# Kernel optimization log

Measured on AMD Instinct MI355X. Metric: run time of the kernel, lower is better.

## Reference

```python
import jax, jax.numpy as jnp
import numpy as np

B, H, W, C = 32, 112, 112, 192
K = 7  # spatial attention conv kernel size


def setup_inputs() -> dict:
    key = jax.random.key(0)
    k1, k2 = jax.random.split(key)
    x = jax.random.normal(k1, (B, H, W, C), dtype=jnp.float32)
    # he_normal init for 7x7 conv with 2 input channels, 1 output channel (HWIO)
    fan_in = K * K * 2
    conv_w = jax.random.normal(k2, (K, K, 2, 1), dtype=jnp.float32) * jnp.sqrt(2.0 / fan_in)
    return {"x": x, "conv_w": conv_w}


def reference(x, conv_w):
    # channel-wise reductions: [B,H,W,1] each
    avg_out = jnp.mean(x, axis=-1, keepdims=True)
    max_out = jnp.max(x, axis=-1, keepdims=True)
    concat = jnp.concatenate([avg_out, max_out], axis=-1)  # [B,H,W,2]
    # 7x7 conv, stride 1, SAME padding, no bias -> [B,H,W,1]
    att = jax.lax.conv_general_dilated(
        concat, conv_w,
        window_strides=(1, 1), padding="SAME",
        dimension_numbers=("NHWC", "HWIO", "NHWC"),
    )
    att = jax.nn.sigmoid(att)
    return x * att  # broadcast multiply back onto full feature map
```

## Files before the change

### kernel.cpp

```cpp
#include <hip/hip_runtime.h>
#include <math.h>

#define B_ 32
#define H_ 112
#define W_ 112
#define C_ 192
#define C4 (C_/4)
#define R_ 7
#define TPI (H_/R_)
#define NBLK (B_*TPI)
#define HALO 3
#define SR (R_ + 2*HALO)
#define SW (W_ + 2*HALO)
#define SWP 120
#define NT_ 1024

typedef float nf4 __attribute__((ext_vector_type(4)));

__global__ __launch_bounds__(NT_, 8) void fused_kernel(const float* __restrict__ x,
                                                       const float* __restrict__ w,
                                                       float* __restrict__ out) {
    __shared__ float2 sm[SR][SWP];
    __shared__ float  sw[98];
    __shared__ float  satt[R_ * W_];

    const int tid = threadIdx.x;
    const int bid = ((int)blockIdx.x & 7) * (NBLK / 8) + ((int)blockIdx.x >> 3);
    const int b   = bid / TPI;
    const int t   = bid - b * TPI;
    const int y0  = t * R_;

    if (tid < 98) sw[tid] = w[tid];
    for (int i = tid; i < SR * SWP; i += NT_)
        ((float2*)sm)[i] = make_float2(0.0f, 0.0f);
    __syncthreads();

    const int g   = tid >> 4;
    const int sub = tid & 15;
    const float* xbase = x + (size_t)(b * H_) * W_ * C_;
    for (int j = 0; j < (SR * W_ + 63) / 64; ++j) {
        const int ps = j * 64 + g;
        if (ps < SR * W_) {
            const int r  = ps / W_;
            const int cl = ps - r * W_;
            const int yy = y0 + r - HALO;
            if (yy >= 0 && yy < H_) {
                const nf4* xp = (const nf4*)(xbase + ((size_t)yy * W_ + cl) * C_);
                nf4 a0 = xp[sub];
                nf4 a1 = xp[sub + 16];
                nf4 a2 = xp[sub + 32];
                float s = ((a0[0]+a0[1]) + (a0[2]+a0[3]))
                        + ((a1[0]+a1[1]) + (a1[2]+a1[3]))
                        + ((a2[0]+a2[1]) + (a2[2]+a2[3]));
                float m0 = fmaxf(fmaxf(a0[0], a0[1]), fmaxf(a0[2], a0[3]));
                float m1 = fmaxf(fmaxf(a1[0], a1[1]), fmaxf(a1[2], a1[3]));
                float m2 = fmaxf(fmaxf(a2[0], a2[1]), fmaxf(a2[2], a2[3]));
                float m  = fmaxf(m0, fmaxf(m1, m2));
                #pragma unroll
                for (int off = 8; off > 0; off >>= 1) {
                    s += __shfl_xor(s, off);
                    m = fmaxf(m, __shfl_xor(m, off));
                }
                if (sub == 0)
                    sm[r][HALO + cl] = make_float2(s * (1.0f / (float)C_), m);
            }
        }
    }
    __syncthreads();

    if (tid < R_ * W_) {
        const int r  = tid / W_;
        const int cl = tid - r * W_;
        float acc = 0.0f;
        #pragma unroll
        for (int ky = 0; ky < 7; ++ky) {
            #pragma unroll
            for (int kx = 0; kx < 7; ++kx) {
                float2 am = sm[r + ky][cl + kx];
                acc = fmaf(am.x, sw[(ky * 7 + kx) * 2 + 0], acc);
                acc = fmaf(am.y, sw[(ky * 7 + kx) * 2 + 1], acc);
            }
        }
        satt[tid] = 1.0f / (1.0f + __expf(-acc));
    }
    __syncthreads();

    const size_t base4 = (size_t)(b * H_ + y0) * W_ * C4;
    const nf4* xr   = (const nf4*)x + base4;
    nf4*       orow = (nf4*)out + base4;
    for (int f = tid; f < R_ * W_ * C4; f += NT_) {
        nf4 v = xr[f];
        v = v * satt[f / C4];
        __builtin_nontemporal_store(v, &orow[f]);
    }
}

extern "C" void kernel_launch(void* const* d_in, const int* in_sizes, int n_in,
                              void* d_out, int out_size, void* d_ws, size_t ws_size,
                              hipStream_t stream) {
    const float* x = (const float*)d_in[0];
    const float* w = (const float*)d_in[1];
    float* out = (float*)d_out;
    fused_kernel<<<NBLK, NT_, 0, stream>>>(x, w, out);
}
```

Before: 173.6 us.

## Split into reduce and apply phases with grid sync to drop halo recompute

```diff
diff --git a/kernel.cpp b/kernel.cpp
--- a/kernel.cpp
+++ b/kernel.cpp
@@ -1,74 +1,86 @@
 #include <hip/hip_runtime.h>
+#include <hip/hip_cooperative_groups.h>
 #include <math.h>
+
+namespace cg = cooperative_groups;
 
 #define B_ 32
 #define H_ 112
 #define W_ 112
 #define C_ 192
 #define C4 (C_/4)
-#define R_ 7
-#define TPI (H_/R_)
-#define NBLK (B_*TPI)
+#define NPOS (B_*H_*W_)
+#define NBLK 1792
+#define RPI (H_/2)
 #define HALO 3
-#define SR (R_ + 2*HALO)
-#define SW (W_ + 2*HALO)
 #define SWP 120
-#define NT_ 1024
 
 typedef float nf4 __attribute__((ext_vector_type(4)));
 
-__global__ __launch_bounds__(NT_, 8) void fused_kernel(const float* __restrict__ x,
-                                                       const float* __restrict__ w,
-                                                       float* __restrict__ out) {
-    __shared__ float2 sm[SR][SWP];
+__device__ __forceinline__ int swz(int raw) { return (raw & 7) * (NBLK / 8) + (raw >> 3); }
+
+__device__ __forceinline__ void phaseA(const float* __restrict__ x,
+                                       float2* __restrict__ ws2, int bid) {
+    const int tid  = threadIdx.x;
+    const int wv   = tid >> 6;
+    const int lane = tid & 63;
+    const int sub  = lane & 15;
+    const int grp  = lane >> 4;
+    const int pbase = bid * 224 + wv * 4 + grp;
+    #pragma unroll
+    for (int it = 0; it < 14; ++it) {
+        const int p = pbase + it * 16;
+        const nf4* xp = (const nf4*)x + (size_t)p * C4;
+        nf4 a0 = __builtin_nontemporal_load(xp + sub);
+        nf4 a1 = __builtin_nontemporal_load(xp + sub + 16);
+        nf4 a2 = __builtin_nontemporal_load(xp + sub + 32);
+        float s = ((a0[0]+a0[1]) + (a0[2]+a0[3]))
+                + ((a1[0]+a1[1]) + (a1[2]+a1[3]))
+                + ((a2[0]+a2[1]) + (a2[2]+a2[3]));
+        float m0 = fmaxf(fmaxf(a0[0], a0[1]), fmaxf(a0[2], a0[3]));
+        float m1 = fmaxf(fmaxf(a1[0], a1[1]), fmaxf(a1[2], a1[3]));
+        float m2 = fmaxf(fmaxf(a2[0], a2[1]), fmaxf(a2[2], a2[3]));
+        float m  = fmaxf(m0, fmaxf(m1, m2));
+        #pragma unroll
+        for (int off = 8; off > 0; off >>= 1) {
+            s += __shfl_xor(s, off);
+            m = fmaxf(m, __shfl_xor(m, off));
+        }
+        if (sub == 0) {
+            float2 r; r.x = s * (1.0f / (float)C_); r.y = m;
+            ws2[p] = r;
+        }
+    }
+}
+
+__device__ __forceinline__ void phaseB(const float* __restrict__ x,
+                                       const float2* __restrict__ ws2,
+                                       const float* __restrict__ w,
+                                       float* __restrict__ out, int bid) {
+    __shared__ float2 sm[2*HALO + 2][SWP];
     __shared__ float  sw[98];
-    __shared__ float  satt[R_ * W_];
+    __shared__ float  satt[2 * W_];
 
     const int tid = threadIdx.x;
-    const int bid = ((int)blockIdx.x & 7) * (NBLK / 8) + ((int)blockIdx.x >> 3);
-    const int b   = bid / TPI;
-    const int t   = bid - b * TPI;
-    const int y0  = t * R_;
+    const int b   = bid / RPI;
+    const int y0  = (bid - b * RPI) * 2;
 
     if (tid < 98) sw[tid] = w[tid];
-    for (int i = tid; i < SR * SWP; i += NT_)
-        ((float2*)sm)[i] = make_float2(0.0f, 0.0f);
-    __syncthreads();
 
-    const int g   = tid >> 4;
-    const int sub = tid & 15;
-    const float* xbase = x + (size_t)(b * H_) * W_ * C_;
-    for (int j = 0; j < (SR * W_ + 63) / 64; ++j) {
-        const int ps = j * 64 + g;
-        if (ps < SR * W_) {
-            const int r  = ps / W_;
-            const int cl = ps - r * W_;
-            const int yy = y0 + r - HALO;
-            if (yy >= 0 && yy < H_) {
-                const nf4* xp = (const nf4*)(xbase + ((size_t)yy * W_ + cl) * C_);
-                nf4 a0 = xp[sub];
-                nf4 a1 = xp[sub + 16];
-                nf4 a2 = xp[sub + 32];
-                float s = ((a0[0]+a0[1]) + (a0[2]+a0[3]))
-                        + ((a1[0]+a1[1]) + (a1[2]+a1[3]))
-                        + ((a2[0]+a2[1]) + (a2[2]+a2[3]));
-                float m0 = fmaxf(fmaxf(a0[0], a0[1]), fmaxf(a0[2], a0[3]));
-                float m1 = fmaxf(fmaxf(a1[0], a1[1]), fmaxf(a1[2], a1[3]));
-                float m2 = fmaxf(fmaxf(a2[0], a2[1]), fmaxf(a2[2], a2[3]));
-                float m  = fmaxf(m0, fmaxf(m1, m2));
-                #pragma unroll
-                for (int off = 8; off > 0; off >>= 1) {
-                    s += __shfl_xor(s, off);
-                    m = fmaxf(m, __shfl_xor(m, off));
-                }
-                if (sub == 0)
-                    sm[r][HALO + cl] = make_float2(s * (1.0f / (float)C_), m);
-            }
-        }
+    const float2* wsb = ws2 + (size_t)b * (H_ * W_);
+    for (int i = tid; i < 8 * (W_ + 2*HALO); i += 256) {
+        const int r  = i / (W_ + 2*HALO);
+        const int c  = i - r * (W_ + 2*HALO);
+        const int yy = y0 + r - HALO;
+        const int xx = c - HALO;
+        float2 v = make_float2(0.0f, 0.0f);
+        if (yy >= 0 && yy < H_ && xx >= 0 && xx < W_)
+            v = wsb[yy * W_ + xx];
+        sm[r][c] = v;
     }
     __syncthreads();
 
-    if (tid < R_ * W_) {
+    if (tid < 2 * W_) {
         const int r  = tid / W_;
         const int cl = tid - r * W_;
         float acc = 0.0f;
@@ -85,14 +97,38 @@
     }
     __syncthreads();
 
-    const size_t base4 = (size_t)(b * H_ + y0) * W_ * C4;
-    const nf4* xr   = (const nf4*)x + base4;
-    nf4*       orow = (nf4*)out + base4;
-    for (int f = tid; f < R_ * W_ * C4; f += NT_) {
-        nf4 v = xr[f];
+    const size_t base4 = ((size_t)b * H_ + y0) * W_ * C4;
+    const nf4* xr = (const nf4*)x + base4;
+    nf4*       o  = (nf4*)out + base4;
+    #pragma unroll 2
+    for (int k = 0; k < (2 * W_ * C4) / 256; ++k) {
+        const int f = tid + k * 256;
+        nf4 v = __builtin_nontemporal_load(xr + f);
         v = v * satt[f / C4];
-        __builtin_nontemporal_store(v, &orow[f]);
+        __builtin_nontemporal_store(v, o + f);
     }
+}
+
+__global__ __launch_bounds__(256, 7) void spatial_coop(const float* __restrict__ x,
+                                                       const float* __restrict__ w,
+                                                       float* __restrict__ out,
+                                                       float2* __restrict__ ws2) {
+    const int bid = swz((int)blockIdx.x);
+    phaseA(x, ws2, bid);
+    __threadfence();
+    cg::this_grid().sync();
+    phaseB(x, ws2, w, out, bid);
+}
+
+__global__ __launch_bounds__(256, 7) void phaseA_kernel(const float* __restrict__ x,
+                                                        float2* __restrict__ ws2) {
+    phaseA(x, ws2, swz((int)blockIdx.x));
+}
+__global__ __launch_bounds__(256, 7) void phaseB_kernel(const float* __restrict__ x,
+                                                        const float2* __restrict__ ws2,
+                                                        const float* __restrict__ w,
+                                                        float* __restrict__ out) {
+    phaseB(x, ws2, w, out, swz((int)blockIdx.x));
 }
 
 extern "C" void kernel_launch(void* const* d_in, const int* in_sizes, int n_in,
@@ -101,5 +137,13 @@
     const float* x = (const float*)d_in[0];
     const float* w = (const float*)d_in[1];
     float* out = (float*)d_out;
-    fused_kernel<<<NBLK, NT_, 0, stream>>>(x, w, out);
+    float2* ws2 = (float2*)d_ws;
+
+    void* args[] = { (void*)&x, (void*)&w, (void*)&out, (void*)&ws2 };
+    hipError_t err = hipLaunchCooperativeKernel((const void*)spatial_coop,
+                                                dim3(NBLK), dim3(256), args, 0, stream);
+    if (err != hipSuccess) {
+        phaseA_kernel<<<NBLK, 256, 0, stream>>>(x, ws2);
+        phaseB_kernel<<<NBLK, 256, 0, stream>>>(x, ws2, w, out);
+    }
 }
```

Measured after the change: 633.5 us. +264.9%, slower.
